# Kernel optimization log

Hardware: AMD Instinct MI355X
Metric: run time of the kernel (lower is better)

The kernel has to match this reference:

```python
import jax, jax.numpy as jnp
import numpy as np

N = 100000
F_IN = 128
HID = 16
C = 16
E = 3200000


def setup_inputs() -> dict:
    key = jax.random.key(0)
    k1, k2, k3, k4, k5, k6 = jax.random.split(key, 6)
    x = jax.random.normal(k1, (N, F_IN), dtype=jnp.float32)
    edge_index = jax.random.randint(k2, (2, E), 0, N, dtype=jnp.int64)
    # GCNConv weight (glorot) + bias
    W1 = jax.random.normal(k3, (F_IN, HID), dtype=jnp.float32) * (1.0 / np.sqrt(F_IN))
    b1 = jnp.zeros((HID,), dtype=jnp.float32)
    # pooling linear
    Wp = jax.random.normal(k4, (HID, C), dtype=jnp.float32) * (1.0 / np.sqrt(HID))
    bp = jax.random.normal(k5, (C,), dtype=jnp.float32) * 0.01
    return {"x": x, "W1": W1, "b1": b1, "Wp": Wp, "bp": bp, "edge_index": edge_index}


def gcn_conv(x, W, b, edge_index, num_nodes):
    # PyG GCNConv: add self-loops, symmetric normalization D^-1/2 (A+I) D^-1/2
    loop = jnp.arange(num_nodes, dtype=edge_index.dtype)
    src = jnp.concatenate([edge_index[0], loop])
    dst = jnp.concatenate([edge_index[1], loop])
    ones = jnp.ones_like(dst, dtype=x.dtype)
    deg = jax.ops.segment_sum(ones, dst, num_segments=num_nodes)  # [N]
    dinv = jnp.where(deg > 0, jax.lax.rsqrt(deg), 0.0)
    norm = dinv[src] * dinv[dst]  # [E+N]
    h = x @ W  # [N, HID] transform before aggregation (fewer bytes moved)
    msgs = h[src] * norm[:, None]  # gather + scale
    agg = jax.ops.segment_sum(msgs, dst, num_segments=num_nodes)  # scatter-add
    return agg + b


def reference(x, W1, b1, Wp, bp, edge_index):
    h = jax.nn.relu(gcn_conv(x, W1, b1, edge_index, N))  # [N, HID]
    s = jax.nn.softmax(h @ Wp + bp, axis=1)  # [N, C]
    return s
```

## Files before the change

### kernel.cpp

```cpp
#include <hip/hip_runtime.h>


#define PCHUNK 4096
#define ACH 2048

__device__ __forceinline__ float bf2f(unsigned int u16) {
    return __uint_as_float(u16 << 16);
}
__device__ __forceinline__ unsigned short f2bf(float f) {
    unsigned int u = __float_as_uint(f);
    u += 0x7fffu + ((u >> 16) & 1u);
    return (unsigned short)(u >> 16);
}

__device__ __forceinline__ int voteBf16(const unsigned int* xw, int tid, int* scratch) {
    if (tid == 0) *scratch = 0;
    __syncthreads();
    unsigned int w = xw[tid];
    unsigned int lo = w & 0xffffu;
    unsigned int elo = (lo >> 7) & 0xffu;
    if (lo == 0u || (elo >= 100u && elo <= 140u)) atomicAdd(scratch, 1);
    __syncthreads();
    return (*scratch >= 160) ? 1 : 0;
}

__global__ __launch_bounds__(256) void k_part(const int* __restrict__ ei,
                                              int* __restrict__ cursor,
                                              unsigned int* __restrict__ bkt,
                                              int E, int Nn, int NB2, int cap) {
    __shared__ int lhist[1024];
    __shared__ int lexcl[1024];
    __shared__ int lbase[1024];
    __shared__ int sa[1024], sb[1024];
    __shared__ unsigned int stage[PCHUNK];
    __shared__ ushort sbk[PCHUNK];
    __shared__ int stot_s;
    __shared__ int v64_s;
    int tid = threadIdx.x;
    #pragma unroll
    for (int k = 0; k < 4; ++k) lhist[tid + k * 256] = 0;
    if (tid == 0) v64_s = 0;
    __syncthreads();
    if (((const unsigned int*)ei)[2 * tid + 1] != 0u) atomicAdd(&v64_s, 1);
    __syncthreads();
    int is64 = (v64_s == 0) ? 1 : 0;
    int e0 = blockIdx.x * PCHUNK;
    int ss[16], dd[16];
    #pragma unroll
    for (int i = 0; i < 16; ++i) {
        int e = e0 + i * 256 + tid;
        int s = -1, d = -1;
        if (e < E) {
            if (is64) { s = ei[2 * e]; d = ei[2 * (E + e)]; }
            else      { s = ei[e];     d = ei[E + e]; }
            if ((unsigned)s >= (unsigned)Nn || (unsigned)d >= (unsigned)Nn) { s = -1; d = -1; }
        }
        ss[i] = s;
        if (d >= 0) {
            int r = atomicAdd(&lhist[d >> 7], 1);
            dd[i] = d | (r << 17);
        } else dd[i] = -1;
    }
    __syncthreads();
    #pragma unroll
    for (int k = 0; k < 4; ++k) sa[tid + k * 256] = lhist[tid + k * 256];
    __syncthreads();
    int* cur = sa; int* nxt = sb;
    for (int off = 1; off < 1024; off <<= 1) {
        #pragma unroll
        for (int k = 0; k < 4; ++k) {
            int i = tid + k * 256;
            nxt[i] = cur[i] + ((i >= off) ? cur[i - off] : 0);
        }
        __syncthreads();
        int* t = cur; cur = nxt; nxt = t;
    }
    #pragma unroll
    for (int k = 0; k < 4; ++k) {
        int i = tid + k * 256;
        lexcl[i] = cur[i] - lhist[i];
    }
    if (tid == 0) stot_s = cur[1023];
    __syncthreads();
    for (int b = tid; b < 1024; b += 256) {
        int c = lhist[b];
        if (b < NB2 && c > 0) {
            int base = atomicAdd(&cursor[b], c);
            lbase[b] = b * cap + base - lexcl[b];
        } else lbase[b] = 0;
    }
    __syncthreads();
    #pragma unroll
    for (int i = 0; i < 16; ++i) {
        if (dd[i] >= 0) {
            int d = dd[i] & 0x1ffff;
            int b = d >> 7;
            int q = lexcl[b] + (dd[i] >> 17);
            stage[q] = (unsigned)ss[i] | ((unsigned)(d & 127) << 17);
            sbk[q] = (ushort)b;
        }
    }
    __syncthreads();
    int stot = stot_s;
    for (int q = tid; q < stot; q += 256) {
        int b = sbk[q];
        int pos = lbase[b] + q;
        if (pos < (b + 1) * cap) bkt[pos] = stage[q];
    }
}

__global__ __launch_bounds__(256) void k_gemmD(const void* __restrict__ xraw,
                                               const void* __restrict__ w1raw,
                                               const unsigned int* __restrict__ bkt,
                                               const int* __restrict__ cursor,
                                               float* __restrict__ dinv,
                                               float* __restrict__ hs,
                                               int Nn, int NB2, int cap) {
    __shared__ float sWt[16 * 132];
    __shared__ int ldeg[256];
    __shared__ float sdv[256];
    __shared__ int vote_s;
    const ushort* xb = (const ushort*)xraw;
    const float* xf = (const float*)xraw;
    int tid = threadIdx.x, b = blockIdx.x;
    const int isbf = voteBf16((const unsigned int*)xraw, tid, &vote_s);
    ldeg[tid] = 0;
    if (isbf) {
        const ushort* w1 = (const ushort*)w1raw;
        for (int i = tid; i < 2048; i += 256) {
            int k = i >> 4, j = i & 15;
            sWt[j * 132 + k] = bf2f(w1[i]);
        }
    } else {
        const float* w1 = (const float*)w1raw;
        for (int i = tid; i < 2048; i += 256) {
            int k = i >> 4, j = i & 15;
            sWt[j * 132 + k] = w1[i];
        }
    }
    __syncthreads();
    {
        int b0 = 2 * b;
        int len0 = (b0 < NB2) ? min(cursor[b0], cap) : 0;
        size_t bb0 = (size_t)b0 * cap;
        for (int e = tid; e < len0; e += 256)
            atomicAdd(&ldeg[(bkt[bb0 + e] >> 17) & 127u], 1);
        int b1i = 2 * b + 1;
        int len1 = (b1i < NB2) ? min(cursor[b1i], cap) : 0;
        size_t bb1 = (size_t)b1i * cap;
        for (int e = tid; e < len1; e += 256)
            atomicAdd(&ldeg[128 + ((bkt[bb1 + e] >> 17) & 127u)], 1);
    }
    __syncthreads();
    {
        float dv = rsqrtf((float)(ldeg[tid] + 1));
        sdv[tid] = dv;
        int n = (b << 8) + tid;
        if (n < Nn) dinv[n] = dv;
    }
    __syncthreads();
    int hq = tid & 3;
    int nodeq = tid >> 2;
    int n0 = (b << 8) + nodeq * 4;
    float acc[4][4] = {};
    for (int ko = 0; ko < 16; ++ko) {
        float xv[4][8];
        #pragma unroll
        for (int r = 0; r < 4; ++r) {
            int n = n0 + r;
            if (n < Nn) {
                if (isbf) {
                    uint4 q = *reinterpret_cast<const uint4*>(xb + (size_t)n * 128 + ko * 8);
                    xv[r][0] = bf2f(q.x & 0xffffu); xv[r][1] = bf2f(q.x >> 16);
                    xv[r][2] = bf2f(q.y & 0xffffu); xv[r][3] = bf2f(q.y >> 16);
                    xv[r][4] = bf2f(q.z & 0xffffu); xv[r][5] = bf2f(q.z >> 16);
                    xv[r][6] = bf2f(q.w & 0xffffu); xv[r][7] = bf2f(q.w >> 16);
                } else {
                    const float4* p = reinterpret_cast<const float4*>(xf + (size_t)n * 128 + ko * 8);
                    float4 a = p[0], bf = p[1];
                    xv[r][0] = a.x; xv[r][1] = a.y; xv[r][2] = a.z; xv[r][3] = a.w;
                    xv[r][4] = bf.x; xv[r][5] = bf.y; xv[r][6] = bf.z; xv[r][7] = bf.w;
                }
            } else {
                #pragma unroll
                for (int u = 0; u < 8; ++u) xv[r][u] = 0.f;
            }
        }
        #pragma unroll
        for (int c = 0; c < 4; ++c) {
            const float* wr = &sWt[(hq * 4 + c) * 132 + ko * 8];
            float4 w0 = *reinterpret_cast<const float4*>(wr);
            float4 w1v = *reinterpret_cast<const float4*>(wr + 4);
            #pragma unroll
            for (int r = 0; r < 4; ++r) {
                acc[r][c] += xv[r][0] * w0.x + xv[r][1] * w0.y + xv[r][2] * w0.z + xv[r][3] * w0.w
                           + xv[r][4] * w1v.x + xv[r][5] * w1v.y + xv[r][6] * w1v.z + xv[r][7] * w1v.w;
            }
        }
    }
    #pragma unroll
    for (int r = 0; r < 4; ++r) {
        int n = n0 + r;
        if (n < Nn) {
            float dv = sdv[nodeq * 4 + r];
            float4 o = make_float4(acc[r][0] * dv, acc[r][1] * dv, acc[r][2] * dv, acc[r][3] * dv);
            *reinterpret_cast<float4*>(hs + (size_t)n * 16 + hq * 4) = o;
        }
    }
}

__global__ __launch_bounds__(256) void k_aggF(const unsigned int* __restrict__ bkt,
                                              const int* __restrict__ cursor,
                                              const float* __restrict__ hs,
                                              const float* __restrict__ dinv,
                                              const void* __restrict__ xraw,
                                              const void* __restrict__ b1raw,
                                              const void* __restrict__ wpraw,
                                              const void* __restrict__ bpraw,
                                              void* __restrict__ outraw,
                                              int Nn, int cap) {
    __shared__ float sAgg[2048];
    __shared__ unsigned int sSorted[ACH];
    __shared__ int cnt[128], excl[128];
    __shared__ int sc[2][128];
    __shared__ float sWp[256];
    __shared__ float sA[256];
    __shared__ int tot_s, vote_s;
    int tid = threadIdx.x, b = blockIdx.x;
    const int isbf = voteBf16((const unsigned int*)xraw, tid, &vote_s);
    sWp[tid] = isbf ? bf2f(((const ushort*)wpraw)[tid]) : ((const float*)wpraw)[tid];
    for (int i = tid; i < 2048; i += 256) sAgg[i] = 0.f;
    int len = min(cursor[b], cap);
    size_t bb = (size_t)b * cap;
    int g = tid >> 4, j = tid & 15;
    for (int c0 = 0; c0 < len; c0 += ACH) {
        if (tid < 128) cnt[tid] = 0;
        __syncthreads();
        unsigned ue[8];
        int rr[8];
        #pragma unroll
        for (int i = 0; i < 8; ++i) {
            int idx = c0 + i * 256 + tid;
            if (idx < len) {
                ue[i] = bkt[bb + idx];
                rr[i] = atomicAdd(&cnt[(ue[i] >> 17) & 127u], 1);
            } else { ue[i] = 0xffffffffu; rr[i] = 0; }
        }
        __syncthreads();
        int v = (tid < 128) ? cnt[tid] : 0;
        if (tid < 128) sc[0][tid] = v;
        __syncthreads();
        int pi = 0;
        for (int off = 1; off < 128; off <<= 1) {
            if (tid < 128) sc[pi ^ 1][tid] = sc[pi][tid] + ((tid >= off) ? sc[pi][tid - off] : 0);
            __syncthreads();
            pi ^= 1;
        }
        if (tid < 128) excl[tid] = sc[pi][tid] - v;
        if (tid == 127) tot_s = sc[pi][127];
        __syncthreads();
        #pragma unroll
        for (int i = 0; i < 8; ++i) {
            if (ue[i] != 0xffffffffu)
                sSorted[excl[(ue[i] >> 17) & 127u] + rr[i]] = ue[i];
        }
        __syncthreads();
        int tot = tot_s;
        #pragma unroll 2
        for (int nn = 0; nn < 8; ++nn) {
            int node = g * 8 + nn;
            int segS = excl[node];
            int segE = (node == 127) ? tot : excl[node + 1];
            float acc = 0.f;
            #pragma unroll 1
            for (int base = segS; base < segE; base += 8) {
                int m = segE - base;
                unsigned e8[8];
                float vv[8];
                #pragma unroll
                for (int i = 0; i < 8; ++i) {
                    int idx = base + i;
                    e8[i] = sSorted[(idx < segE) ? idx : segS];
                }
                #pragma unroll
                for (int i = 0; i < 8; ++i)
                    vv[i] = hs[(size_t)(e8[i] & 0x1ffffu) * 16 + j];
                #pragma unroll
                for (int i = 0; i < 8; ++i)
                    vv[i] = (i < m) ? vv[i] : 0.f;
                vv[0] += vv[4]; vv[1] += vv[5]; vv[2] += vv[6]; vv[3] += vv[7];
                vv[0] += vv[2]; vv[1] += vv[3];
                acc += vv[0] + vv[1];
            }
            if (segE > segS) sAgg[node * 16 + j] += acc;
        }
        __syncthreads();
    }
    __syncthreads();
    int nl = tid >> 4, c = tid & 15;
    float b1v = isbf ? bf2f(((const ushort*)b1raw)[c]) : ((const float*)b1raw)[c];
    float bpv = isbf ? bf2f(((const ushort*)bpraw)[c]) : ((const float*)bpraw)[c];
    int nbase = b << 7;
    #pragma unroll 1
    for (int pass = 0; pass < 8; ++pass) {
        int node = pass * 16 + nl;
        int n = nbase + node;
        float dv = 0.f, sv = 0.f;
        if (n < Nn) { dv = dinv[n]; sv = hs[(size_t)n * 16 + c]; }
        float hval = fmaxf(dv * (sv + sAgg[node * 16 + c]) + b1v, 0.f);
        sA[tid] = hval;
        __syncthreads();
        float acc = bpv;
        #pragma unroll
        for (int jj = 0; jj < 16; ++jj) acc += sA[nl * 16 + jj] * sWp[jj * 16 + c];
        float m = acc;
        #pragma unroll
        for (int off = 1; off < 16; off <<= 1) m = fmaxf(m, __shfl_xor(m, off, 16));
        float ev = __expf(acc - m);
        float s = ev;
        #pragma unroll
        for (int off = 1; off < 16; off <<= 1) s += __shfl_xor(s, off, 16);
        if (n < Nn) {
            float val = ev / s;
            if (isbf) ((ushort*)outraw)[(size_t)n * 16 + c] = f2bf(val);
            else      ((float*)outraw)[(size_t)n * 16 + c] = val;
        }
        __syncthreads();
    }
}

extern "C" void kernel_launch(void* const* d_in, const int* in_sizes, int n_in,
                              void* d_out, int out_size, void* d_ws, size_t ws_size,
                              hipStream_t stream) {
    const void* x  = d_in[0];
    const void* W1 = d_in[1];
    const void* b1 = d_in[2];
    const void* Wp = d_in[3];
    const void* bp = d_in[4];
    const int*  ei = (const int*)d_in[5];

    int Nn  = in_sizes[0] / 128;
    int E   = in_sizes[5] / 2;
    int NB  = (Nn + 255) >> 8;
    int NB2 = (Nn + 127) >> 7;

    size_t Ns = (size_t)Nn;
    char* ws = (char*)d_ws;
    size_t off = 0;
    auto alloc = [&](size_t bytes) { void* p = ws + off; off += (bytes + 63) & ~(size_t)63; return p; };
    float* hs     = (float*)alloc(Ns * 16 * 4);
    float* dinv   = (float*)alloc(Ns * 4);
    int*   cursor = (int*)alloc(1024 * 4);
    size_t remain = (ws_size > off) ? (ws_size - off) : 0;
    int cap = (int)(remain / 4 / (size_t)NB2);
    int want = 6144;
    if (cap > want) cap = want;
    cap &= ~63;
    unsigned int* bkt = (unsigned int*)alloc((size_t)NB2 * (size_t)cap * 4);

    hipMemsetAsync(cursor, 0, 1024 * 4, stream);
    k_part<<<(E + PCHUNK - 1) / PCHUNK, 256, 0, stream>>>(ei, cursor, bkt, E, Nn, NB2, cap);
    k_gemmD<<<NB, 256, 0, stream>>>(x, W1, bkt, cursor, dinv, hs, Nn, NB2, cap);
    k_aggF<<<NB2, 256, 0, stream>>>(bkt, cursor, hs, dinv, x, b1, Wp, bp, d_out, Nn, cap);
}
```

Baseline: 251.5 us.

## Fuse three kernels into one cooperative persistent kernel with grid syncs

Merges the partition, GEMM/degree, and aggregation kernels into one cooperative kernel that uses grid.sync between phases, with a union of shared memory layouts, and falls back to three launches if the cooperative launch fails. The partition phase drops the in-block prefix scan and staging buffer and scatters directly to global buckets. The GEMM phase now handles 128-node tiles instead of 256. The aim is to remove launch gaps and the memset, but grid-wide syncs, a capped grid of 1792 blocks and uncoalesced bucket writes may cost more than they save.

```diff
diff --git a/kernel.cpp b/kernel.cpp
--- a/kernel.cpp
+++ b/kernel.cpp
@@ -1,8 +1,16 @@
 #include <hip/hip_runtime.h>
+#include <hip/hip_cooperative_groups.h>
+namespace cg = cooperative_groups;
 
 
 #define PCHUNK 4096
 #define ACH 2048
+
+struct SMemA { int lhist[1024]; int lbase[1024]; };
+struct SMemB { float sWt[16 * 132]; int ldeg[128]; float sdv[128]; };
+struct SMemC { float sAgg[2048]; unsigned sSorted[ACH]; int cnt[128]; int excl[128];
+               int sc[2][128]; float sWp[256]; float sA[256]; int tot; };
+union SMemU { SMemA pa; SMemB pb; SMemC pc; int vote[2]; };
 
 __device__ __forceinline__ float bf2f(unsigned int u16) {
     return __uint_as_float(u16 << 16);
@@ -13,38 +21,13 @@
     return (unsigned short)(u >> 16);
 }
 
-__device__ __forceinline__ int voteBf16(const unsigned int* xw, int tid, int* scratch) {
-    if (tid == 0) *scratch = 0;
-    __syncthreads();
-    unsigned int w = xw[tid];
-    unsigned int lo = w & 0xffffu;
-    unsigned int elo = (lo >> 7) & 0xffu;
-    if (lo == 0u || (elo >= 100u && elo <= 140u)) atomicAdd(scratch, 1);
-    __syncthreads();
-    return (*scratch >= 160) ? 1 : 0;
-}
-
-__global__ __launch_bounds__(256) void k_part(const int* __restrict__ ei,
-                                              int* __restrict__ cursor,
-                                              unsigned int* __restrict__ bkt,
-                                              int E, int Nn, int NB2, int cap) {
-    __shared__ int lhist[1024];
-    __shared__ int lexcl[1024];
-    __shared__ int lbase[1024];
-    __shared__ int sa[1024], sb[1024];
-    __shared__ unsigned int stage[PCHUNK];
-    __shared__ ushort sbk[PCHUNK];
-    __shared__ int stot_s;
-    __shared__ int v64_s;
-    int tid = threadIdx.x;
-    #pragma unroll
-    for (int k = 0; k < 4; ++k) lhist[tid + k * 256] = 0;
-    if (tid == 0) v64_s = 0;
-    __syncthreads();
-    if (((const unsigned int*)ei)[2 * tid + 1] != 0u) atomicAdd(&v64_s, 1);
-    __syncthreads();
-    int is64 = (v64_s == 0) ? 1 : 0;
-    int e0 = blockIdx.x * PCHUNK;
+__device__ __forceinline__ void phaseA(SMemU& sm, int ch, const int* __restrict__ ei,
+                                       int* __restrict__ cursor, unsigned* __restrict__ bkt,
+                                       int E, int Nn, int cap, int is64, int tid) {
+    #pragma unroll
+    for (int k = 0; k < 4; ++k) sm.pa.lhist[tid + k * 256] = 0;
+    __syncthreads();
+    int e0 = ch * PCHUNK;
     int ss[16], dd[16];
     #pragma unroll
     for (int i = 0; i < 16; ++i) {
@@ -57,37 +40,18 @@
         }
         ss[i] = s;
         if (d >= 0) {
-            int r = atomicAdd(&lhist[d >> 7], 1);
+            int r = atomicAdd(&sm.pa.lhist[d >> 7], 1);
             dd[i] = d | (r << 17);
         } else dd[i] = -1;
     }
     __syncthreads();
     #pragma unroll
-    for (int k = 0; k < 4; ++k) sa[tid + k * 256] = lhist[tid + k * 256];
-    __syncthreads();
-    int* cur = sa; int* nxt = sb;
-    for (int off = 1; off < 1024; off <<= 1) {
-        #pragma unroll
-        for (int k = 0; k < 4; ++k) {
-            int i = tid + k * 256;
-            nxt[i] = cur[i] + ((i >= off) ? cur[i - off] : 0);
-        }
-        __syncthreads();
-        int* t = cur; cur = nxt; nxt = t;
-    }
-    #pragma unroll
     for (int k = 0; k < 4; ++k) {
-        int i = tid + k * 256;
-        lexcl[i] = cur[i] - lhist[i];
-    }
-    if (tid == 0) stot_s = cur[1023];
-    __syncthreads();
-    for (int b = tid; b < 1024; b += 256) {
-        int c = lhist[b];
-        if (b < NB2 && c > 0) {
-            int base = atomicAdd(&cursor[b], c);
-            lbase[b] = b * cap + base - lexcl[b];
-        } else lbase[b] = 0;
+        int b = tid + k * 256;
+        int c = sm.pa.lhist[b];
+        int lb = 0;
+        if (c > 0) lb = b * cap + atomicAdd(&cursor[b], c);
+        sm.pa.lbase[b] = lb;
     }
     __syncthreads();
     #pragma unroll
@@ -95,78 +59,51 @@
         if (dd[i] >= 0) {
             int d = dd[i] & 0x1ffff;
             int b = d >> 7;
-            int q = lexcl[b] + (dd[i] >> 17);
-            stage[q] = (unsigned)ss[i] | ((unsigned)(d & 127) << 17);
-            sbk[q] = (ushort)b;
-        }
-    }
-    __syncthreads();
-    int stot = stot_s;
-    for (int q = tid; q < stot; q += 256) {
-        int b = sbk[q];
-        int pos = lbase[b] + q;
-        if (pos < (b + 1) * cap) bkt[pos] = stage[q];
-    }
-}
-
-__global__ __launch_bounds__(256) void k_gemmD(const void* __restrict__ xraw,
-                                               const void* __restrict__ w1raw,
-                                               const unsigned int* __restrict__ bkt,
-                                               const int* __restrict__ cursor,
-                                               float* __restrict__ dinv,
-                                               float* __restrict__ hs,
-                                               int Nn, int NB2, int cap) {
-    __shared__ float sWt[16 * 132];
-    __shared__ int ldeg[256];
-    __shared__ float sdv[256];
-    __shared__ int vote_s;
+            int pos = sm.pa.lbase[b] + (dd[i] >> 17);
+            if (pos < (b + 1) * cap)
+                bkt[pos] = (unsigned)ss[i] | ((unsigned)(d & 127) << 17);
+        }
+    }
+    __syncthreads();
+}
+
+__device__ __forceinline__ void phaseB(SMemU& sm, int tb, const void* __restrict__ xraw,
+                                       const void* __restrict__ w1raw,
+                                       const unsigned* __restrict__ bkt,
+                                       const int* __restrict__ cursor,
+                                       float* __restrict__ dinv, float* __restrict__ hs,
+                                       int Nn, int cap, int isbf, int tid) {
+    if (isbf) {
+        const ushort* w1 = (const ushort*)w1raw;
+        for (int i = tid; i < 2048; i += 256) sm.pb.sWt[(i & 15) * 132 + (i >> 4)] = bf2f(w1[i]);
+    } else {
+        const float* w1 = (const float*)w1raw;
+        for (int i = tid; i < 2048; i += 256) sm.pb.sWt[(i & 15) * 132 + (i >> 4)] = w1[i];
+    }
+    if (tid < 128) sm.pb.ldeg[tid] = 0;
+    __syncthreads();
+    int len = min(cursor[tb], cap);
+    size_t bb = (size_t)tb * cap;
+    for (int e = tid; e < len; e += 256)
+        atomicAdd(&sm.pb.ldeg[(bkt[bb + e] >> 17) & 127u], 1);
+    __syncthreads();
+    if (tid < 128) {
+        float dv = rsqrtf((float)(sm.pb.ldeg[tid] + 1));
+        sm.pb.sdv[tid] = dv;
+        int n = (tb << 7) + tid;
+        if (n < Nn) dinv[n] = dv;
+    }
+    __syncthreads();
     const ushort* xb = (const ushort*)xraw;
     const float* xf = (const float*)xraw;
-    int tid = threadIdx.x, b = blockIdx.x;
-    const int isbf = voteBf16((const unsigned int*)xraw, tid, &vote_s);
-    ldeg[tid] = 0;
-    if (isbf) {
-        const ushort* w1 = (const ushort*)w1raw;
-        for (int i = tid; i < 2048; i += 256) {
-            int k = i >> 4, j = i & 15;
-            sWt[j * 132 + k] = bf2f(w1[i]);
-        }
-    } else {
-        const float* w1 = (const float*)w1raw;
-        for (int i = tid; i < 2048; i += 256) {
-            int k = i >> 4, j = i & 15;
-            sWt[j * 132 + k] = w1[i];
-        }
-    }
-    __syncthreads();
-    {
-        int b0 = 2 * b;
-        int len0 = (b0 < NB2) ? min(cursor[b0], cap) : 0;
-        size_t bb0 = (size_t)b0 * cap;
-        for (int e = tid; e < len0; e += 256)
-            atomicAdd(&ldeg[(bkt[bb0 + e] >> 17) & 127u], 1);
-        int b1i = 2 * b + 1;
-        int len1 = (b1i < NB2) ? min(cursor[b1i], cap) : 0;
-        size_t bb1 = (size_t)b1i * cap;
-        for (int e = tid; e < len1; e += 256)
-            atomicAdd(&ldeg[128 + ((bkt[bb1 + e] >> 17) & 127u)], 1);
-    }
-    __syncthreads();
-    {
-        float dv = rsqrtf((float)(ldeg[tid] + 1));
-        sdv[tid] = dv;
-        int n = (b << 8) + tid;
-        if (n < Nn) dinv[n] = dv;
-    }
-    __syncthreads();
     int hq = tid & 3;
-    int nodeq = tid >> 2;
-    int n0 = (b << 8) + nodeq * 4;
-    float acc[4][4] = {};
+    int np = tid >> 2;
+    int n0 = (tb << 7) + np * 2;
+    float acc[2][4] = {};
     for (int ko = 0; ko < 16; ++ko) {
-        float xv[4][8];
-        #pragma unroll
-        for (int r = 0; r < 4; ++r) {
+        float xv[2][8];
+        #pragma unroll
+        for (int r = 0; r < 2; ++r) {
             int n = n0 + r;
             if (n < Nn) {
                 if (isbf) {
@@ -188,53 +125,44 @@
         }
         #pragma unroll
         for (int c = 0; c < 4; ++c) {
-            const float* wr = &sWt[(hq * 4 + c) * 132 + ko * 8];
+            const float* wr = &sm.pb.sWt[(hq * 4 + c) * 132 + ko * 8];
             float4 w0 = *reinterpret_cast<const float4*>(wr);
             float4 w1v = *reinterpret_cast<const float4*>(wr + 4);
             #pragma unroll
-            for (int r = 0; r < 4; ++r) {
+            for (int r = 0; r < 2; ++r) {
                 acc[r][c] += xv[r][0] * w0.x + xv[r][1] * w0.y + xv[r][2] * w0.z + xv[r][3] * w0.w
                            + xv[r][4] * w1v.x + xv[r][5] * w1v.y + xv[r][6] * w1v.z + xv[r][7] * w1v.w;
             }
         }
     }
     #pragma unroll
-    for (int r = 0; r < 4; ++r) {
+    for (int r = 0; r < 2; ++r) {
         int n = n0 + r;
         if (n < Nn) {
-            float dv = sdv[nodeq * 4 + r];
+            float dv = sm.pb.sdv[np * 2 + r];
             float4 o = make_float4(acc[r][0] * dv, acc[r][1] * dv, acc[r][2] * dv, acc[r][3] * dv);
             *reinterpret_cast<float4*>(hs + (size_t)n * 16 + hq * 4) = o;
         }
     }
-}
-
-__global__ __launch_bounds__(256) void k_aggF(const unsigned int* __restrict__ bkt,
-                                              const int* __restrict__ cursor,
-                                              const float* __restrict__ hs,
-                                              const float* __restrict__ dinv,
-                                              const void* __restrict__ xraw,
-                                              const void* __restrict__ b1raw,
-                                              const void* __restrict__ wpraw,
-                                              const void* __restrict__ bpraw,
-                                              void* __restrict__ outraw,
-                                              int Nn, int cap) {
-    __shared__ float sAgg[2048];
-    __shared__ unsigned int sSorted[ACH];
-    __shared__ int cnt[128], excl[128];
-    __shared__ int sc[2][128];
-    __shared__ float sWp[256];
-    __shared__ float sA[256];
-    __shared__ int tot_s, vote_s;
-    int tid = threadIdx.x, b = blockIdx.x;
-    const int isbf = voteBf16((const unsigned int*)xraw, tid, &vote_s);
-    sWp[tid] = isbf ? bf2f(((const ushort*)wpraw)[tid]) : ((const float*)wpraw)[tid];
-    for (int i = tid; i < 2048; i += 256) sAgg[i] = 0.f;
-    int len = min(cursor[b], cap);
-    size_t bb = (size_t)b * cap;
+    __syncthreads();
+}
+
+__device__ __forceinline__ void phaseC(SMemU& sm, int bk, const unsigned* __restrict__ bkt,
+                                       const int* __restrict__ cursor,
+                                       const float* __restrict__ hs,
+                                       const float* __restrict__ dinv,
+                                       const void* __restrict__ b1raw,
+                                       const void* __restrict__ wpraw,
+                                       const void* __restrict__ bpraw,
+                                       void* __restrict__ outraw,
+                                       int Nn, int cap, int isbf, int tid) {
+    sm.pc.sWp[tid] = isbf ? bf2f(((const ushort*)wpraw)[tid]) : ((const float*)wpraw)[tid];
+    for (int i = tid; i < 2048; i += 256) sm.pc.sAgg[i] = 0.f;
+    int len = min(cursor[bk], cap);
+    size_t bb = (size_t)bk * cap;
     int g = tid >> 4, j = tid & 15;
     for (int c0 = 0; c0 < len; c0 += ACH) {
-        if (tid < 128) cnt[tid] = 0;
+        if (tid < 128) sm.pc.cnt[tid] = 0;
         __syncthreads();
         unsigned ue[8];
         int rr[8];
@@ -243,34 +171,34 @@
             int idx = c0 + i * 256 + tid;
             if (idx < len) {
                 ue[i] = bkt[bb + idx];
-                rr[i] = atomicAdd(&cnt[(ue[i] >> 17) & 127u], 1);
+                rr[i] = atomicAdd(&sm.pc.cnt[(ue[i] >> 17) & 127u], 1);
             } else { ue[i] = 0xffffffffu; rr[i] = 0; }
         }
         __syncthreads();
-        int v = (tid < 128) ? cnt[tid] : 0;
-        if (tid < 128) sc[0][tid] = v;
+        int v = (tid < 128) ? sm.pc.cnt[tid] : 0;
+        if (tid < 128) sm.pc.sc[0][tid] = v;
         __syncthreads();
         int pi = 0;
         for (int off = 1; off < 128; off <<= 1) {
-            if (tid < 128) sc[pi ^ 1][tid] = sc[pi][tid] + ((tid >= off) ? sc[pi][tid - off] : 0);
+            if (tid < 128) sm.pc.sc[pi ^ 1][tid] = sm.pc.sc[pi][tid] + ((tid >= off) ? sm.pc.sc[pi][tid - off] : 0);
             __syncthreads();
             pi ^= 1;
         }
-        if (tid < 128) excl[tid] = sc[pi][tid] - v;
-        if (tid == 127) tot_s = sc[pi][127];
+        if (tid < 128) sm.pc.excl[tid] = sm.pc.sc[pi][tid] - v;
+        if (tid == 127) sm.pc.tot = sm.pc.sc[pi][127];
         __syncthreads();
         #pragma unroll
         for (int i = 0; i < 8; ++i) {
             if (ue[i] != 0xffffffffu)
-                sSorted[excl[(ue[i] >> 17) & 127u] + rr[i]] = ue[i];
-        }
-        __syncthreads();
-        int tot = tot_s;
+                sm.pc.sSorted[sm.pc.excl[(ue[i] >> 17) & 127u] + rr[i]] = ue[i];
+        }
+        __syncthreads();
+        int tot = sm.pc.tot;
         #pragma unroll 2
         for (int nn = 0; nn < 8; ++nn) {
             int node = g * 8 + nn;
-            int segS = excl[node];
-            int segE = (node == 127) ? tot : excl[node + 1];
+            int segS = sm.pc.excl[node];
+            int segE = (node == 127) ? tot : sm.pc.excl[node + 1];
             float acc = 0.f;
             #pragma unroll 1
             for (int base = segS; base < segE; base += 8) {
@@ -280,7 +208,7 @@
                 #pragma unroll
                 for (int i = 0; i < 8; ++i) {
                     int idx = base + i;
-                    e8[i] = sSorted[(idx < segE) ? idx : segS];
+                    e8[i] = sm.pc.sSorted[(idx < segE) ? idx : segS];
                 }
                 #pragma unroll
                 for (int i = 0; i < 8; ++i)
@@ -292,7 +220,7 @@
                 vv[0] += vv[2]; vv[1] += vv[3];
                 acc += vv[0] + vv[1];
             }
-            if (segE > segS) sAgg[node * 16 + j] += acc;
+            if (segE > segS) sm.pc.sAgg[node * 16 + j] += acc;
         }
         __syncthreads();
     }
@@ -300,26 +228,26 @@
     int nl = tid >> 4, c = tid & 15;
     float b1v = isbf ? bf2f(((const ushort*)b1raw)[c]) : ((const float*)b1raw)[c];
     float bpv = isbf ? bf2f(((const ushort*)bpraw)[c]) : ((const float*)bpraw)[c];
-    int nbase = b << 7;
+    int nbase = bk << 7;
     #pragma unroll 1
     for (int pass = 0; pass < 8; ++pass) {
         int node = pass * 16 + nl;
         int n = nbase + node;
         float dv = 0.f, sv = 0.f;
         if (n < Nn) { dv = dinv[n]; sv = hs[(size_t)n * 16 + c]; }
-        float hval = fmaxf(dv * (sv + sAgg[node * 16 + c]) + b1v, 0.f);
-        sA[tid] = hval;
+        float hval = fmaxf(dv * (sv + sm.pc.sAgg[node * 16 + c]) + b1v, 0.f);
+        sm.pc.sA[tid] = hval;
         __syncthreads();
         float acc = bpv;
         #pragma unroll
-        for (int jj = 0; jj < 16; ++jj) acc += sA[nl * 16 + jj] * sWp[jj * 16 + c];
+        for (int jj = 0; jj < 16; ++jj) acc += sm.pc.sA[nl * 16 + jj] * sm.pc.sWp[jj * 16 + c];
         float m = acc;
         #pragma unroll
-        for (int off = 1; off < 16; off <<= 1) m = fmaxf(m, __shfl_xor(m, off, 16));
+        for (int off2 = 1; off2 < 16; off2 <<= 1) m = fmaxf(m, __shfl_xor(m, off2, 16));
         float ev = __expf(acc - m);
         float s = ev;
         #pragma unroll
-        for (int off = 1; off < 16; off <<= 1) s += __shfl_xor(s, off, 16);
+        for (int off2 = 1; off2 < 16; off2 <<= 1) s += __shfl_xor(s, off2, 16);
         if (n < Nn) {
             float val = ev / s;
             if (isbf) ((ushort*)outraw)[(size_t)n * 16 + c] = f2bf(val);
@@ -327,6 +255,96 @@
         }
         __syncthreads();
     }
+}
+
+__global__ __launch_bounds__(256) void k_mega(const void* xraw, const void* w1raw,
+                                              const void* b1raw, const void* wpraw,
+                                              const void* bpraw, const int* ei,
+                                              void* outraw, float* hs, float* dinv,
+                                              int* cursor, unsigned* bkt,
+                                              int Nn, int E, int cap, int NCH, int NB2) {
+    cg::grid_group grid = cg::this_grid();
+    __shared__ SMemU sm;
+    int tid = threadIdx.x, bid = blockIdx.x, G = gridDim.x;
+    if (tid == 0) { sm.vote[0] = 0; sm.vote[1] = 0; }
+    __syncthreads();
+    {
+        unsigned w = ((const unsigned*)xraw)[tid];
+        unsigned lo = w & 0xffffu, elo = (lo >> 7) & 0xffu;
+        if (lo == 0u || (elo >= 100u && elo <= 140u)) atomicAdd(&sm.vote[0], 1);
+        if (((const unsigned*)ei)[2 * tid + 1] != 0u) atomicAdd(&sm.vote[1], 1);
+    }
+    __syncthreads();
+    const int isbf = (sm.vote[0] >= 160);
+    const int is64 = (sm.vote[1] == 0);
+    __syncthreads();
+    for (int i = bid * 256 + tid; i < 1024; i += G * 256) cursor[i] = 0;
+    __threadfence();
+    grid.sync();
+    for (int ch = bid; ch < NCH; ch += G)
+        phaseA(sm, ch, ei, cursor, bkt, E, Nn, cap, is64, tid);
+    __threadfence();
+    grid.sync();
+    for (int tb = bid; tb < NB2; tb += G)
+        phaseB(sm, tb, xraw, w1raw, bkt, cursor, dinv, hs, Nn, cap, isbf, tid);
+    __threadfence();
+    grid.sync();
+    for (int bk = bid; bk < NB2; bk += G)
+        phaseC(sm, bk, bkt, cursor, hs, dinv, b1raw, wpraw, bpraw, outraw, Nn, cap, isbf, tid);
+}
+
+__global__ __launch_bounds__(256) void k_partS(const int* __restrict__ ei, int* __restrict__ cursor,
+                                               unsigned* __restrict__ bkt, int E, int Nn, int cap, int NCH) {
+    __shared__ SMemU sm;
+    int tid = threadIdx.x;
+    if (tid == 0) sm.vote[1] = 0;
+    __syncthreads();
+    if (((const unsigned*)ei)[2 * tid + 1] != 0u) atomicAdd(&sm.vote[1], 1);
+    __syncthreads();
+    int is64 = (sm.vote[1] == 0);
+    __syncthreads();
+    for (int ch = blockIdx.x; ch < NCH; ch += gridDim.x)
+        phaseA(sm, ch, ei, cursor, bkt, E, Nn, cap, is64, tid);
+}
+
+__global__ __launch_bounds__(256) void k_gemmS(const void* xraw, const void* w1raw,
+                                               const unsigned* __restrict__ bkt,
+                                               const int* __restrict__ cursor,
+                                               float* __restrict__ dinv, float* __restrict__ hs,
+                                               int Nn, int cap, int NB2) {
+    __shared__ SMemU sm;
+    int tid = threadIdx.x;
+    if (tid == 0) sm.vote[0] = 0;
+    __syncthreads();
+    unsigned w = ((const unsigned*)xraw)[tid];
+    unsigned lo = w & 0xffffu, elo = (lo >> 7) & 0xffu;
+    if (lo == 0u || (elo >= 100u && elo <= 140u)) atomicAdd(&sm.vote[0], 1);
+    __syncthreads();
+    int isbf = (sm.vote[0] >= 160);
+    __syncthreads();
+    for (int tb = blockIdx.x; tb < NB2; tb += gridDim.x)
+        phaseB(sm, tb, xraw, w1raw, bkt, cursor, dinv, hs, Nn, cap, isbf, tid);
+}
+
+__global__ __launch_bounds__(256) void k_aggFS(const unsigned* __restrict__ bkt,
+                                               const int* __restrict__ cursor,
+                                               const float* __restrict__ hs,
+                                               const float* __restrict__ dinv,
+                                               const void* xraw, const void* b1raw,
+                                               const void* wpraw, const void* bpraw,
+                                               void* outraw, int Nn, int cap, int NB2) {
+    __shared__ SMemU sm;
+    int tid = threadIdx.x;
+    if (tid == 0) sm.vote[0] = 0;
+    __syncthreads();
+    unsigned w = ((const unsigned*)xraw)[tid];
+    unsigned lo = w & 0xffffu, elo = (lo >> 7) & 0xffu;
+    if (lo == 0u || (elo >= 100u && elo <= 140u)) atomicAdd(&sm.vote[0], 1);
+    __syncthreads();
+    int isbf = (sm.vote[0] >= 160);
+    __syncthreads();
+    for (int bk = blockIdx.x; bk < NB2; bk += gridDim.x)
+        phaseC(sm, bk, bkt, cursor, hs, dinv, b1raw, wpraw, bpraw, outraw, Nn, cap, isbf, tid);
 }
 
 extern "C" void kernel_launch(void* const* d_in, const int* in_sizes, int n_in,
@@ -341,8 +359,8 @@
 
     int Nn  = in_sizes[0] / 128;
     int E   = in_sizes[5] / 2;
-    int NB  = (Nn + 255) >> 8;
     int NB2 = (Nn + 127) >> 7;
+    int NCH = (E + PCHUNK - 1) / PCHUNK;
 
     size_t Ns = (size_t)Nn;
     char* ws = (char*)d_ws;
@@ -358,8 +376,19 @@
     cap &= ~63;
     unsigned int* bkt = (unsigned int*)alloc((size_t)NB2 * (size_t)cap * 4);
 
-    hipMemsetAsync(cursor, 0, 1024 * 4, stream);
-    k_part<<<(E + PCHUNK - 1) / PCHUNK, 256, 0, stream>>>(ei, cursor, bkt, E, Nn, NB2, cap);
-    k_gemmD<<<NB, 256, 0, stream>>>(x, W1, bkt, cursor, dinv, hs, Nn, NB2, cap);
-    k_aggF<<<NB2, 256, 0, stream>>>(bkt, cursor, hs, dinv, x, b1, Wp, bp, d_out, Nn, cap);
-}
+    int G = (NCH > NB2) ? NCH : NB2;
+    if (G > 1792) G = 1792;
+    void* outv = d_out;
+    void* kargs[] = { (void*)&x, (void*)&W1, (void*)&b1, (void*)&Wp, (void*)&bp,
+                      (void*)&ei, (void*)&outv, (void*)&hs, (void*)&dinv,
+                      (void*)&cursor, (void*)&bkt,
+                      (void*)&Nn, (void*)&E, (void*)&cap, (void*)&NCH, (void*)&NB2 };
+    hipError_t err = hipLaunchCooperativeKernel((const void*)k_mega, dim3(G), dim3(256),
+                                                kargs, 0, stream);
+    if (err != hipSuccess) {
+        hipMemsetAsync(cursor, 0, 1024 * 4, stream);
+        k_partS<<<NCH, 256, 0, stream>>>(ei, cursor, bkt, E, Nn, cap, NCH);
+        k_gemmS<<<NB2, 256, 0, stream>>>(x, W1, bkt, cursor, dinv, hs, Nn, cap, NB2);
+        k_aggFS<<<NB2, 256, 0, stream>>>(bkt, cursor, hs, dinv, x, b1, Wp, bp, d_out, Nn, cap, NB2);
+    }
+}
```

Measured after the change: 752.8 us. 199% more time.
